# Kernel optimization log

Measured on AMD Instinct MI355X. Metric: run time of the kernel, lower is better.

Reference implementation:

```python
import math
import jax, jax.numpy as jnp
import numpy as np

B, T, D, H, L = 8, 512, 128, 128, 2
W_SCALE = 0.05  # xavier-like small init to keep exp() input gate numerically sane


def setup_inputs() -> dict:
    key = jax.random.key(0)
    ks = jax.random.split(key, 14)
    inp = {"x": jax.random.normal(ks[0], (B, T, D), jnp.float32)}
    names_w = ["Wq", "Wk", "Wv", "Wi", "Wf", "Wo"]
    for j, nm in enumerate(names_w):
        inp[nm] = jax.random.normal(ks[1 + j], (L, H, D), jnp.float32) * W_SCALE
    # q/k/v biases zero-initialized per reset_parameters; gate biases random
    inp["bq"] = jnp.zeros((L, H), jnp.float32)
    inp["bk"] = jnp.zeros((L, H), jnp.float32)
    inp["bv"] = jnp.zeros((L, H), jnp.float32)
    inp["bi"] = jax.random.normal(ks[7], (L, H), jnp.float32) * W_SCALE
    inp["bf"] = jax.random.normal(ks[8], (L, H), jnp.float32) * W_SCALE
    inp["bo"] = jax.random.normal(ks[9], (L, H), jnp.float32) * W_SCALE
    return inp


def _mlstm_layer(xin, Wq, bq, Wk, bk, Wv, bv, Wi, bi, Wf, bf, Wo, bo):
    # xin: (B, T, Din). Precompute all 6 projections for the full sequence.
    q = jnp.einsum("btd,hd->bth", xin, Wq) + bq
    k = (jnp.einsum("btd,hd->bth", xin, Wk) + bk) * (1.0 / math.sqrt(H))
    v = jnp.einsum("btd,hd->bth", xin, Wv) + bv
    i = jnp.exp(jnp.einsum("btd,hd->bth", xin, Wi) + bi)
    f = jax.nn.sigmoid(jnp.einsum("btd,hd->bth", xin, Wf) + bf)
    o = jax.nn.sigmoid(jnp.einsum("btd,hd->bth", xin, Wo) + bo)

    def step(carry, qkvifo):
        C, n = carry                      # C: (B,H,H), n: (B,H)
        qt, kt, vt, it, ft, ot = qkvifo   # each (B,H)
        h_tilde = jnp.einsum("bij,bj->bi", C, qt)
        denom = jnp.maximum(jnp.abs(jnp.einsum("bi,bi->b", n, qt)), 1.0)[:, None]
        h = ot * (h_tilde / denom)
        n_new = ft * n + it * kt
        C_new = ft[:, :, None] * C + it[:, :, None] * (vt[:, :, None] * kt[:, None, :])
        return (C_new, n_new), h

    Bc = xin.shape[0]
    C0 = jnp.zeros((Bc, H, H), xin.dtype)
    n0 = jnp.zeros((Bc, H), xin.dtype)
    seq = tuple(jnp.swapaxes(a, 0, 1) for a in (q, k, v, i, f, o))  # (T,B,H)
    _, hs = jax.lax.scan(step, (C0, n0), seq)
    return jnp.swapaxes(hs, 0, 1)  # (B,T,H)


def reference(x, Wq, bq, Wk, bk, Wv, bv, Wi, bi, Wf, bf, Wo, bo):
    h = x
    for l in range(L):  # small fixed layer loop (dropout=0.0 -> identity)
        h = _mlstm_layer(h, Wq[l], bq[l], Wk[l], bk[l], Wv[l], bv[l],
                         Wi[l], bi[l], Wf[l], bf[l], Wo[l], bo[l])
    return h  # (B, T, H) output sequence of last layer
```

## Files before the change

### kernel.cpp

```cpp
#include <hip/hip_runtime.h>
#include <math.h>

#define BB 8
#define TT 512
#define DD 128
#define HH 128
#define BT_ (BB * TT)
#define CL 64
#define NCH 8
static const size_t BTH = (size_t)BT_ * HH;


struct WArgs { const float* W[6]; };
struct BArgs { const float* b[6]; };

template <int CTRL>
__device__ __forceinline__ float dpp_add(float x) {
  int y = __builtin_amdgcn_update_dpp(0, __builtin_bit_cast(int, x), CTRL,
                                      0xF, 0xF, true);
  return x + __builtin_bit_cast(float, y);
}

template <int CTRL>
__device__ __forceinline__ float dpp_mov(float old, float x) {
  int y = __builtin_amdgcn_update_dpp(__builtin_bit_cast(int, old),
                                      __builtin_bit_cast(int, x), CTRL,
                                      0xF, 0xF, false);
  return __builtin_bit_cast(float, y);
}

__device__ __forceinline__ float rd_lane(float x, int l) {
  return __builtin_bit_cast(
      float, __builtin_amdgcn_readlane(__builtin_bit_cast(int, x), l));
}

__global__ __launch_bounds__(256)
void transpose_w(WArgs w, float* __restrict__ Wt) {
  __shared__ float t[32][33];
  const int l = blockIdx.y / 6, p = blockIdx.y % 6;
  const float* src = w.W[p] + (size_t)l * HH * DD;
  float* dst = Wt + (size_t)blockIdx.y * HH * DD;
  const int ty0 = (blockIdx.x >> 2) * 32, tx0 = (blockIdx.x & 3) * 32;
  const int tx = threadIdx.x & 31, ty = threadIdx.x >> 5;
#pragma unroll
  for (int j = 0; j < 32; j += 8)
    t[ty + j][tx] = src[(size_t)(ty0 + ty + j) * DD + tx0 + tx];
  __syncthreads();
#pragma unroll
  for (int j = 0; j < 32; j += 8)
    dst[(size_t)(tx0 + ty + j) * HH + ty0 + tx] = t[tx][ty + j];
}

__global__ __launch_bounds__(256)
void proj_kernel(const float* __restrict__ X, const float* __restrict__ Wtl,
                 BArgs args, float* __restrict__ act) {
  __shared__ float xs[32][132];
  const int p = blockIdx.y;
  const int row0 = blockIdx.x * 32;
  const int tid = threadIdx.x;
  {
    const float4* xg = (const float4*)(X + (size_t)row0 * DD);
#pragma unroll
    for (int i = 0; i < 4; ++i) {
      int u = tid + 256 * i;
      float4 v = xg[u];
      *(float4*)&xs[u >> 5][(u & 31) * 4] = v;
    }
  }
  __syncthreads();

  const int h0 = (tid & 15) * 8;
  const int r0 = (tid >> 4) * 2;
  const float* wtp = Wtl + (size_t)p * HH * DD;

  float acc[2][8];
#pragma unroll
  for (int r = 0; r < 2; ++r)
#pragma unroll
    for (int j = 0; j < 8; ++j) acc[r][j] = 0.f;

  for (int d0 = 0; d0 < DD; d0 += 4) {
    float4 wa[4], wb[4];
#pragma unroll
    for (int i = 0; i < 4; ++i) {
      wa[i] = *(const float4*)(wtp + (size_t)(d0 + i) * HH + h0);
      wb[i] = *(const float4*)(wtp + (size_t)(d0 + i) * HH + h0 + 4);
    }
    float4 x0 = *(const float4*)&xs[r0][d0];
    float4 x1 = *(const float4*)&xs[r0 + 1][d0];
    const float xa[4] = {x0.x, x0.y, x0.z, x0.w};
    const float xb[4] = {x1.x, x1.y, x1.z, x1.w};
#pragma unroll
    for (int i = 0; i < 4; ++i) {
      acc[0][0] = fmaf(xa[i], wa[i].x, acc[0][0]);
      acc[0][1] = fmaf(xa[i], wa[i].y, acc[0][1]);
      acc[0][2] = fmaf(xa[i], wa[i].z, acc[0][2]);
      acc[0][3] = fmaf(xa[i], wa[i].w, acc[0][3]);
      acc[0][4] = fmaf(xa[i], wb[i].x, acc[0][4]);
      acc[0][5] = fmaf(xa[i], wb[i].y, acc[0][5]);
      acc[0][6] = fmaf(xa[i], wb[i].z, acc[0][6]);
      acc[0][7] = fmaf(xa[i], wb[i].w, acc[0][7]);
      acc[1][0] = fmaf(xb[i], wa[i].x, acc[1][0]);
      acc[1][1] = fmaf(xb[i], wa[i].y, acc[1][1]);
      acc[1][2] = fmaf(xb[i], wa[i].z, acc[1][2]);
      acc[1][3] = fmaf(xb[i], wa[i].w, acc[1][3]);
      acc[1][4] = fmaf(xb[i], wb[i].x, acc[1][4]);
      acc[1][5] = fmaf(xb[i], wb[i].y, acc[1][5]);
      acc[1][6] = fmaf(xb[i], wb[i].z, acc[1][6]);
      acc[1][7] = fmaf(xb[i], wb[i].w, acc[1][7]);
    }
  }

  const float4 b0 = *(const float4*)(args.b[p] + h0);
  const float4 b1 = *(const float4*)(args.b[p] + h0 + 4);
  const float bias[8] = {b0.x, b0.y, b0.z, b0.w, b1.x, b1.y, b1.z, b1.w};
#pragma unroll
  for (int r = 0; r < 2; ++r) {
    const size_t row = (size_t)row0 + r0 + r;
    float v[8];
#pragma unroll
    for (int j = 0; j < 8; ++j) {
      float a = acc[r][j] + bias[j];
      if (p == 1)      a *= 0.088388347648318447f;
      else if (p == 3) a = __expf(a);
      else if (p >= 4) a = 1.0f / (1.0f + __expf(-a));
      v[j] = a;
    }
    if (p == 0) {
      float* dst = act + row * HH + h0;
      *(float4*)dst = make_float4(v[0], v[1], v[2], v[3]);
      *(float4*)(dst + 4) = make_float4(v[4], v[5], v[6], v[7]);
    } else if (p == 1) {
      float* dst = act + BTH + row * HH + h0;
      *(float4*)dst = make_float4(v[0], v[1], v[2], v[3]);
      *(float4*)(dst + 4) = make_float4(v[4], v[5], v[6], v[7]);
    } else if (p == 3 || p == 4) {
      float* dst = act + 2 * BTH + row * 2 * HH + 2 * h0 + (p == 3 ? 0 : 1);
#pragma unroll
      for (int j = 0; j < 8; ++j) dst[2 * j] = v[j];
    } else {
      float* dst = act + 4 * BTH + row * 2 * HH + 2 * h0 + (p == 2 ? 0 : 1);
#pragma unroll
      for (int j = 0; j < 8; ++j) dst[2 * j] = v[j];
    }
  }
}

__global__ __launch_bounds__(128)
void nseg_kernel(const float* __restrict__ act, float* __restrict__ segAB) {
  const int b = blockIdx.x & 7, seg = blockIdx.x >> 3;
  const int p = threadIdx.x;
  const size_t boff = (size_t)b * TT * HH;
  const float* kp = act + BTH + boff + p;
  const float* ifp = act + 2 * BTH + 2 * boff + 2 * p;
  const int t0 = seg * 8;
  float A = 1.f, Bv = 0.f;
#pragma unroll
  for (int j = 0; j < 8; ++j) {
    const float2 iff = *(const float2*)(ifp + (size_t)(t0 + j) * 2 * HH);
    const float kv = kp[(size_t)(t0 + j) * HH];
    A *= iff.y;
    Bv = fmaf(iff.y, Bv, iff.x * kv);
  }
  *(float2*)(segAB + ((size_t)(b * 128 + p) * 64 + seg) * 2) =
      make_float2(A, Bv);
}

__global__ __launch_bounds__(64)
void nsum_kernel(const float* __restrict__ segAB, float* __restrict__ nstart) {
  const int chain = blockIdx.x;
  const int lane = threadIdx.x;
  const float2 ab = *(const float2*)(segAB + ((size_t)chain * 64 + lane) * 2);
  float A = ab.x, Bv = ab.y;
#define SCAN_LVL(CTRL)                          \
  {                                             \
    float As = dpp_mov<CTRL>(1.0f, A);          \
    float Bs = dpp_mov<CTRL>(0.0f, Bv);         \
    Bv = fmaf(A, Bs, Bv);                       \
    A = A * As;                                 \
  }
  SCAN_LVL(0x111)
  SCAN_LVL(0x112)
  SCAN_LVL(0x114)
  SCAN_LVL(0x118)
  SCAN_LVL(0x142)
  SCAN_LVL(0x143)
#undef SCAN_LVL
  const int idx = (lane + 1) & 63;
  nstart[(size_t)chain * 64 + idx] = (lane == 63) ? 0.f : Bv;
}

__global__ __launch_bounds__(128)
void nexp_denom_kernel(float* __restrict__ act,
                       const float* __restrict__ nstart) {
  __shared__ float pl[8][132];
  __shared__ float den[8];
  const int b = blockIdx.x & 7, seg = blockIdx.x >> 3;
  const int p = threadIdx.x;
  const size_t boff = (size_t)b * TT * HH;
  const float* qp = act + boff + p;
  const float* kp = act + BTH + boff + p;
  const float* ifp = act + 2 * BTH + 2 * boff + 2 * p;
  const int t0 = seg * 8;
  float n = nstart[(size_t)(b * 128 + p) * 64 + seg];
  float prod[8];
#pragma unroll
  for (int j = 0; j < 8; ++j) {
    const float2 iff = *(const float2*)(ifp + (size_t)(t0 + j) * 2 * HH);
    const float kv = kp[(size_t)(t0 + j) * HH];
    const float qv = qp[(size_t)(t0 + j) * HH];
    prod[j] = n * qv;
    n = fmaf(iff.y, n, iff.x * kv);
  }
#pragma unroll
  for (int j = 0; j < 8; ++j) pl[j][p] = prod[j];
  __syncthreads();
  {
    const int j = p >> 4, c = p & 15;
    const float4 a = *(const float4*)&pl[j][c * 8];
    const float4 d = *(const float4*)&pl[j][c * 8 + 4];
    float s = ((a.x + a.y) + (a.z + a.w)) + ((d.x + d.y) + (d.z + d.w));
    s = dpp_add<0x111>(s);
    s = dpp_add<0x112>(s);
    s = dpp_add<0x114>(s);
    s = dpp_add<0x118>(s);
    if ((p & 15) == 15)
      den[j] = __builtin_amdgcn_rcpf(fmaxf(fabsf(s), 1.0f));
  }
  __syncthreads();
  float* vop = act + 4 * BTH + 2 * boff;
#pragma unroll
  for (int j = 0; j < 8; ++j)
    vop[(size_t)(t0 + j) * 2 * HH + 2 * p + 1] *= den[j];
}

__global__ __launch_bounds__(512)
void cseg2_kernel(const float* __restrict__ act, float* __restrict__ cbuf,
                  float* __restrict__ abuf) {
  __shared__ __align__(16) float kt[CL][128];
  __shared__ __align__(16) float ift[CL][64];
  __shared__ __align__(16) float vot[CL][64];
  const int tid = threadIdx.x;
  const int lane = tid & 63, wid = tid >> 6;
  const int blk = blockIdx.x;
  const int b = blk & 7, ch = (blk >> 3) & 7, qtr = blk >> 6;
  const int t0 = ch * CL;
  const int p0 = qtr * 32;
  const size_t boff = (size_t)b * TT * HH;
  const float* kg = act + BTH + boff;
  const float* ifg = act + 2 * BTH + 2 * boff;
  const float* vog = act + 4 * BTH + 2 * boff;

#pragma unroll
  for (int i = 0; i < 4; ++i) {
    const int u = tid + 512 * i;
    const int r = u >> 5, c = (u & 31) * 4;
    *(float4*)&kt[r][c] = *(const float4*)(kg + (size_t)(t0 + r) * HH + c);
  }
#pragma unroll
  for (int i = 0; i < 2; ++i) {
    const int u = tid + 512 * i;
    const int r = u >> 4, c = (u & 15) * 4;
    *(float4*)&ift[r][c] =
        *(const float4*)(ifg + (size_t)(t0 + r) * 2 * HH + 2 * p0 + c);
    *(float4*)&vot[r][c] =
        *(const float4*)(vog + (size_t)(t0 + r) * 2 * HH + 2 * p0 + c);
  }
  __syncthreads();

  const int pl = lane >> 4, cl = lane & 15;
  const int plocal = wid * 4 + pl;
  const int p = p0 + plocal;

  float C[8];
#pragma unroll
  for (int j = 0; j < 8; ++j) C[j] = 0.f;
  float Af = 1.f;

#pragma unroll 4
  for (int t = 0; t < CL; ++t) {
    const float2 gif = *(const float2*)&ift[t][2 * plocal];
    const float2 gvo = *(const float2*)&vot[t][2 * plocal];
    const float4 k0 = *(const float4*)&kt[t][cl * 4];
    const float4 k1 = *(const float4*)&kt[t][cl * 4 + 64];
    const float a = gif.x * gvo.x;
    const float f = gif.y;
    C[0] = fmaf(f, C[0], a * k0.x);
    C[1] = fmaf(f, C[1], a * k0.y);
    C[2] = fmaf(f, C[2], a * k0.z);
    C[3] = fmaf(f, C[3], a * k0.w);
    C[4] = fmaf(f, C[4], a * k1.x);
    C[5] = fmaf(f, C[5], a * k1.y);
    C[6] = fmaf(f, C[6], a * k1.z);
    C[7] = fmaf(f, C[7], a * k1.w);
    Af *= f;
  }

  const size_t slot = (size_t)(b * 128 + p) * NCH + ch;
  *(float4*)(cbuf + slot * 128 + cl * 4) = make_float4(C[0], C[1], C[2], C[3]);
  *(float4*)(cbuf + slot * 128 + cl * 4 + 64) =
      make_float4(C[4], C[5], C[6], C[7]);
  if (cl == 0) abuf[slot] = Af;
}

__global__ __launch_bounds__(64)
void ccomb_kernel(float* __restrict__ cbuf, const float* __restrict__ abuf) {
  const int chain = blockIdx.x;
  const int lane = threadIdx.x;
  const float av = abuf[(size_t)chain * 8 + (lane & 7)];
  float Cs0 = 0.f, Cs1 = 0.f;
#pragma unroll
  for (int g = 0; g < 8; ++g) {
    float* ptr = cbuf + ((size_t)chain * 8 + g) * 128 + 2 * lane;
    const float2 Bv = *(const float2*)ptr;
    const float Ag = rd_lane(av, g);
    *(float2*)ptr = make_float2(Cs0, Cs1);
    Cs0 = fmaf(Ag, Cs0, Bv.x);
    Cs1 = fmaf(Ag, Cs1, Bv.y);
  }
}

__global__ __launch_bounds__(512)
void hscan2_kernel(const float* __restrict__ act, float* __restrict__ hout,
                   const float* __restrict__ cbuf) {
  __shared__ __align__(16) float qt[CL][128];
  __shared__ __align__(16) float kt[CL][128];
  __shared__ __align__(16) float ift[CL][64];
  __shared__ __align__(16) float vot[CL][64];
  const int tid = threadIdx.x;
  const int lane = tid & 63, wid = tid >> 6;
  const int blk = blockIdx.x;
  const int b = blk & 7, ch = (blk >> 3) & 7, qtr = blk >> 6;
  const int t0 = ch * CL;
  const int p0 = qtr * 32;
  const size_t boff = (size_t)b * TT * HH;
  const float* qg = act + boff;
  const float* kg = act + BTH + boff;
  const float* ifg = act + 2 * BTH + 2 * boff;
  const float* vog = act + 4 * BTH + 2 * boff;

#pragma unroll
  for (int i = 0; i < 4; ++i) {
    const int u = tid + 512 * i;
    const int r = u >> 5, c = (u & 31) * 4;
    *(float4*)&qt[r][c] = *(const float4*)(qg + (size_t)(t0 + r) * HH + c);
    *(float4*)&kt[r][c] = *(const float4*)(kg + (size_t)(t0 + r) * HH + c);
  }
#pragma unroll
  for (int i = 0; i < 2; ++i) {
    const int u = tid + 512 * i;
    const int r = u >> 4, c = (u & 15) * 4;
    *(float4*)&ift[r][c] =
        *(const float4*)(ifg + (size_t)(t0 + r) * 2 * HH + 2 * p0 + c);
    *(float4*)&vot[r][c] =
        *(const float4*)(vog + (size_t)(t0 + r) * 2 * HH + 2 * p0 + c);
  }
  __syncthreads();

  const int pl = lane >> 4, cl = lane & 15;
  const int plocal = wid * 4 + pl;
  const int p = p0 + plocal;

  float C[8];
  {
    const size_t slot = (size_t)(b * 128 + p) * NCH + ch;
    const float4 c0 = *(const float4*)(cbuf + slot * 128 + cl * 4);
    const float4 c1 = *(const float4*)(cbuf + slot * 128 + cl * 4 + 64);
    C[0] = c0.x; C[1] = c0.y; C[2] = c0.z; C[3] = c0.w;
    C[4] = c1.x; C[5] = c1.y; C[6] = c1.z; C[7] = c1.w;
  }
  float* hbase = hout + boff + p;

#pragma unroll 4
  for (int t = 0; t < CL; ++t) {
    const float2 gif = *(const float2*)&ift[t][2 * plocal];
    const float2 gvo = *(const float2*)&vot[t][2 * plocal];
    const float4 q0 = *(const float4*)&qt[t][cl * 4];
    const float4 q1 = *(const float4*)&qt[t][cl * 4 + 64];
    const float4 k0 = *(const float4*)&kt[t][cl * 4];
    const float4 k1 = *(const float4*)&kt[t][cl * 4 + 64];
    float s0 = C[0] * q0.x;
    float s1 = C[4] * q1.x;
    s0 = fmaf(C[1], q0.y, s0);
    s1 = fmaf(C[5], q1.y, s1);
    s0 = fmaf(C[2], q0.z, s0);
    s1 = fmaf(C[6], q1.z, s1);
    s0 = fmaf(C[3], q0.w, s0);
    s1 = fmaf(C[7], q1.w, s1);
    float s = s0 + s1;
    const float a = gif.x * gvo.x;
    const float f = gif.y;
    C[0] = fmaf(f, C[0], a * k0.x);
    C[1] = fmaf(f, C[1], a * k0.y);
    C[2] = fmaf(f, C[2], a * k0.z);
    C[3] = fmaf(f, C[3], a * k0.w);
    C[4] = fmaf(f, C[4], a * k1.x);
    C[5] = fmaf(f, C[5], a * k1.y);
    C[6] = fmaf(f, C[6], a * k1.z);
    C[7] = fmaf(f, C[7], a * k1.w);
    s = dpp_add<0x111>(s);
    s = dpp_add<0x112>(s);
    s = dpp_add<0x114>(s);
    s = dpp_add<0x118>(s);
    if (cl == 15) hbase[(size_t)(t0 + t) * HH] = s * gvo.y;
  }
}

extern "C" void kernel_launch(void* const* d_in, const int* in_sizes, int n_in,
                              void* d_out, int out_size, void* d_ws,
                              size_t ws_size, hipStream_t stream) {
  (void)in_sizes; (void)n_in; (void)out_size; (void)ws_size;
  const float* x = (const float*)d_in[0];
  float* act = (float*)d_ws;
  float* hbuf = act + 6 * BTH;
  float* cbuf = act + 7 * BTH;
  float* abuf = cbuf + (size_t)1024 * 8 * 128;
  float* Wt = (float*)d_out;
  float* segAB = Wt + 196608;
  float* nstart = Wt + 327680;

  WArgs wa;
  for (int j = 0; j < 6; ++j) wa.W[j] = (const float*)d_in[1 + j];
  transpose_w<<<dim3(16, 12), 256, 0, stream>>>(wa, Wt);

  for (int l = 0; l < 2; ++l) {
    BArgs ba;
    for (int j = 0; j < 6; ++j)
      ba.b[j] = (const float*)d_in[7 + j] + (size_t)l * HH;
    const float* wtl = Wt + (size_t)l * 6 * HH * DD;
    const float* xin = (l == 0) ? x : hbuf;
    float* hdst = (l == 0) ? hbuf : (float*)d_out;
    proj_kernel<<<dim3(BT_ / 32, 6), 256, 0, stream>>>(xin, wtl, ba, act);
    nseg_kernel<<<512, 128, 0, stream>>>(act, segAB);
    nsum_kernel<<<1024, 64, 0, stream>>>(segAB, nstart);
    nexp_denom_kernel<<<512, 128, 0, stream>>>(act, nstart);
    cseg2_kernel<<<256, 512, 0, stream>>>(act, cbuf, abuf);
    ccomb_kernel<<<1024, 64, 0, stream>>>(cbuf, abuf);
    hscan2_kernel<<<256, 512, 0, stream>>>(act, hdst, cbuf);
  }
}
```

Measured before the change: 220.5 us.

## Fold normalizer scan into chunk pass and inline cross-chunk state combine

Halves the chunk length so the chunk-local C and hidden-state scans launch twice as many blocks. The n-state chunk summary is computed inside the C-chunk kernel, and a single ndenom kernel combines the chunk prefixes and computes the denominators, replacing three separate n kernels. The ccomb kernel is dropped: each hscan block rebuilds its starting C by serially folding all earlier chunk states. This cuts launches per layer from six to three, at the cost of redundant prefix work that grows with chunk index and a low-parallelism ndenom kernel with serial loops.

```diff
diff --git a/kernel.cpp b/kernel.cpp
--- a/kernel.cpp
+++ b/kernel.cpp
@@ -6,8 +6,8 @@
 #define DD 128
 #define HH 128
 #define BT_ (BB * TT)
-#define CL 64
-#define NCH 8
+#define CL 32
+#define NCH 16
 static const size_t BTH = (size_t)BT_ * HH;
 
 
@@ -19,19 +19,6 @@
   int y = __builtin_amdgcn_update_dpp(0, __builtin_bit_cast(int, x), CTRL,
                                       0xF, 0xF, true);
   return x + __builtin_bit_cast(float, y);
-}
-
-template <int CTRL>
-__device__ __forceinline__ float dpp_mov(float old, float x) {
-  int y = __builtin_amdgcn_update_dpp(__builtin_bit_cast(int, old),
-                                      __builtin_bit_cast(int, x), CTRL,
-                                      0xF, 0xF, false);
-  return __builtin_bit_cast(float, y);
-}
-
-__device__ __forceinline__ float rd_lane(float x, int l) {
-  return __builtin_bit_cast(
-      float, __builtin_amdgcn_readlane(__builtin_bit_cast(int, x), l));
 }
 
 __global__ __launch_bounds__(256)
@@ -146,104 +133,16 @@
   }
 }
 
-__global__ __launch_bounds__(128)
-void nseg_kernel(const float* __restrict__ act, float* __restrict__ segAB) {
-  const int b = blockIdx.x & 7, seg = blockIdx.x >> 3;
-  const int p = threadIdx.x;
-  const size_t boff = (size_t)b * TT * HH;
-  const float* kp = act + BTH + boff + p;
-  const float* ifp = act + 2 * BTH + 2 * boff + 2 * p;
-  const int t0 = seg * 8;
-  float A = 1.f, Bv = 0.f;
-#pragma unroll
-  for (int j = 0; j < 8; ++j) {
-    const float2 iff = *(const float2*)(ifp + (size_t)(t0 + j) * 2 * HH);
-    const float kv = kp[(size_t)(t0 + j) * HH];
-    A *= iff.y;
-    Bv = fmaf(iff.y, Bv, iff.x * kv);
-  }
-  *(float2*)(segAB + ((size_t)(b * 128 + p) * 64 + seg) * 2) =
-      make_float2(A, Bv);
-}
-
-__global__ __launch_bounds__(64)
-void nsum_kernel(const float* __restrict__ segAB, float* __restrict__ nstart) {
-  const int chain = blockIdx.x;
-  const int lane = threadIdx.x;
-  const float2 ab = *(const float2*)(segAB + ((size_t)chain * 64 + lane) * 2);
-  float A = ab.x, Bv = ab.y;
-#define SCAN_LVL(CTRL)                          \
-  {                                             \
-    float As = dpp_mov<CTRL>(1.0f, A);          \
-    float Bs = dpp_mov<CTRL>(0.0f, Bv);         \
-    Bv = fmaf(A, Bs, Bv);                       \
-    A = A * As;                                 \
-  }
-  SCAN_LVL(0x111)
-  SCAN_LVL(0x112)
-  SCAN_LVL(0x114)
-  SCAN_LVL(0x118)
-  SCAN_LVL(0x142)
-  SCAN_LVL(0x143)
-#undef SCAN_LVL
-  const int idx = (lane + 1) & 63;
-  nstart[(size_t)chain * 64 + idx] = (lane == 63) ? 0.f : Bv;
-}
-
-__global__ __launch_bounds__(128)
-void nexp_denom_kernel(float* __restrict__ act,
-                       const float* __restrict__ nstart) {
-  __shared__ float pl[8][132];
-  __shared__ float den[8];
-  const int b = blockIdx.x & 7, seg = blockIdx.x >> 3;
-  const int p = threadIdx.x;
-  const size_t boff = (size_t)b * TT * HH;
-  const float* qp = act + boff + p;
-  const float* kp = act + BTH + boff + p;
-  const float* ifp = act + 2 * BTH + 2 * boff + 2 * p;
-  const int t0 = seg * 8;
-  float n = nstart[(size_t)(b * 128 + p) * 64 + seg];
-  float prod[8];
-#pragma unroll
-  for (int j = 0; j < 8; ++j) {
-    const float2 iff = *(const float2*)(ifp + (size_t)(t0 + j) * 2 * HH);
-    const float kv = kp[(size_t)(t0 + j) * HH];
-    const float qv = qp[(size_t)(t0 + j) * HH];
-    prod[j] = n * qv;
-    n = fmaf(iff.y, n, iff.x * kv);
-  }
-#pragma unroll
-  for (int j = 0; j < 8; ++j) pl[j][p] = prod[j];
-  __syncthreads();
-  {
-    const int j = p >> 4, c = p & 15;
-    const float4 a = *(const float4*)&pl[j][c * 8];
-    const float4 d = *(const float4*)&pl[j][c * 8 + 4];
-    float s = ((a.x + a.y) + (a.z + a.w)) + ((d.x + d.y) + (d.z + d.w));
-    s = dpp_add<0x111>(s);
-    s = dpp_add<0x112>(s);
-    s = dpp_add<0x114>(s);
-    s = dpp_add<0x118>(s);
-    if ((p & 15) == 15)
-      den[j] = __builtin_amdgcn_rcpf(fmaxf(fabsf(s), 1.0f));
-  }
-  __syncthreads();
-  float* vop = act + 4 * BTH + 2 * boff;
-#pragma unroll
-  for (int j = 0; j < 8; ++j)
-    vop[(size_t)(t0 + j) * 2 * HH + 2 * p + 1] *= den[j];
-}
-
 __global__ __launch_bounds__(512)
 void cseg2_kernel(const float* __restrict__ act, float* __restrict__ cbuf,
-                  float* __restrict__ abuf) {
+                  float* __restrict__ abuf, float* __restrict__ nbufB) {
   __shared__ __align__(16) float kt[CL][128];
   __shared__ __align__(16) float ift[CL][64];
   __shared__ __align__(16) float vot[CL][64];
   const int tid = threadIdx.x;
   const int lane = tid & 63, wid = tid >> 6;
   const int blk = blockIdx.x;
-  const int b = blk & 7, ch = (blk >> 3) & 7, qtr = blk >> 6;
+  const int b = blk & 7, ch = (blk >> 3) & (NCH - 1), qtr = blk >> 7;
   const int t0 = ch * CL;
   const int p0 = qtr * 32;
   const size_t boff = (size_t)b * TT * HH;
@@ -252,15 +151,13 @@
   const float* vog = act + 4 * BTH + 2 * boff;
 
 #pragma unroll
-  for (int i = 0; i < 4; ++i) {
+  for (int i = 0; i < CL / 16; ++i) {
     const int u = tid + 512 * i;
     const int r = u >> 5, c = (u & 31) * 4;
     *(float4*)&kt[r][c] = *(const float4*)(kg + (size_t)(t0 + r) * HH + c);
   }
-#pragma unroll
-  for (int i = 0; i < 2; ++i) {
-    const int u = tid + 512 * i;
-    const int r = u >> 4, c = (u & 15) * 4;
+  {
+    const int r = tid >> 4, c = (tid & 15) * 4;
     *(float4*)&ift[r][c] =
         *(const float4*)(ifg + (size_t)(t0 + r) * 2 * HH + 2 * p0 + c);
     *(float4*)&vot[r][c] =
@@ -275,7 +172,7 @@
   float C[8];
 #pragma unroll
   for (int j = 0; j < 8; ++j) C[j] = 0.f;
-  float Af = 1.f;
+  float Af = 1.f, Bn = 0.f;
 
 #pragma unroll 4
   for (int t = 0; t < CL; ++t) {
@@ -283,6 +180,7 @@
     const float2 gvo = *(const float2*)&vot[t][2 * plocal];
     const float4 k0 = *(const float4*)&kt[t][cl * 4];
     const float4 k1 = *(const float4*)&kt[t][cl * 4 + 64];
+    const float kp = kt[t][p];
     const float a = gif.x * gvo.x;
     const float f = gif.y;
     C[0] = fmaf(f, C[0], a * k0.x);
@@ -294,35 +192,75 @@
     C[6] = fmaf(f, C[6], a * k1.z);
     C[7] = fmaf(f, C[7], a * k1.w);
     Af *= f;
+    Bn = fmaf(f, Bn, gif.x * kp);
   }
 
   const size_t slot = (size_t)(b * 128 + p) * NCH + ch;
   *(float4*)(cbuf + slot * 128 + cl * 4) = make_float4(C[0], C[1], C[2], C[3]);
   *(float4*)(cbuf + slot * 128 + cl * 4 + 64) =
       make_float4(C[4], C[5], C[6], C[7]);
-  if (cl == 0) abuf[slot] = Af;
-}
-
-__global__ __launch_bounds__(64)
-void ccomb_kernel(float* __restrict__ cbuf, const float* __restrict__ abuf) {
-  const int chain = blockIdx.x;
-  const int lane = threadIdx.x;
-  const float av = abuf[(size_t)chain * 8 + (lane & 7)];
-  float Cs0 = 0.f, Cs1 = 0.f;
-#pragma unroll
-  for (int g = 0; g < 8; ++g) {
-    float* ptr = cbuf + ((size_t)chain * 8 + g) * 128 + 2 * lane;
-    const float2 Bv = *(const float2*)ptr;
-    const float Ag = rd_lane(av, g);
-    *(float2*)ptr = make_float2(Cs0, Cs1);
-    Cs0 = fmaf(Ag, Cs0, Bv.x);
-    Cs1 = fmaf(Ag, Cs1, Bv.y);
+  if (cl == 0) {
+    abuf[slot] = Af;
+    nbufB[slot] = Bn;
+  }
+}
+
+__global__ __launch_bounds__(128)
+void ndenom_kernel(float* __restrict__ act, const float* __restrict__ abuf,
+                   const float* __restrict__ nbufB) {
+  __shared__ float plds[8][132];
+  __shared__ float den[8];
+  const int b = blockIdx.x & 7, ch = blockIdx.x >> 3;
+  const int p = threadIdx.x;
+  const size_t boff = (size_t)b * TT * HH;
+  const float* qp = act + boff + p;
+  const float* kp = act + BTH + boff + p;
+  const float* ifp = act + 2 * BTH + 2 * boff + 2 * p;
+  float* vop = act + 4 * BTH + 2 * boff;
+  const size_t cb = (size_t)(b * 128 + p) * NCH;
+
+  float n = 0.f;
+#pragma unroll 1
+  for (int g = 0; g < ch; ++g) n = fmaf(abuf[cb + g], n, nbufB[cb + g]);
+
+#pragma unroll 1
+  for (int grp = 0; grp < CL / 8; ++grp) {
+    const int t0 = ch * CL + grp * 8;
+    float prod[8];
+#pragma unroll
+    for (int j = 0; j < 8; ++j) {
+      const float2 iff = *(const float2*)(ifp + (size_t)(t0 + j) * 2 * HH);
+      const float kv = kp[(size_t)(t0 + j) * HH];
+      const float qv = qp[(size_t)(t0 + j) * HH];
+      prod[j] = n * qv;
+      n = fmaf(iff.y, n, iff.x * kv);
+    }
+#pragma unroll
+    for (int j = 0; j < 8; ++j) plds[j][p] = prod[j];
+    __syncthreads();
+    {
+      const int j = p >> 4, c = p & 15;
+      const float4 a = *(const float4*)&plds[j][c * 8];
+      const float4 d = *(const float4*)&plds[j][c * 8 + 4];
+      float s = ((a.x + a.y) + (a.z + a.w)) + ((d.x + d.y) + (d.z + d.w));
+      s = dpp_add<0x111>(s);
+      s = dpp_add<0x112>(s);
+      s = dpp_add<0x114>(s);
+      s = dpp_add<0x118>(s);
+      if ((p & 15) == 15)
+        den[j] = __builtin_amdgcn_rcpf(fmaxf(fabsf(s), 1.0f));
+    }
+    __syncthreads();
+#pragma unroll
+    for (int j = 0; j < 8; ++j)
+      vop[(size_t)(t0 + j) * 2 * HH + 2 * p + 1] *= den[j];
   }
 }
 
 __global__ __launch_bounds__(512)
 void hscan2_kernel(const float* __restrict__ act, float* __restrict__ hout,
-                   const float* __restrict__ cbuf) {
+                   const float* __restrict__ cbuf,
+                   const float* __restrict__ abuf) {
   __shared__ __align__(16) float qt[CL][128];
   __shared__ __align__(16) float kt[CL][128];
   __shared__ __align__(16) float ift[CL][64];
@@ -330,7 +268,7 @@
   const int tid = threadIdx.x;
   const int lane = tid & 63, wid = tid >> 6;
   const int blk = blockIdx.x;
-  const int b = blk & 7, ch = (blk >> 3) & 7, qtr = blk >> 6;
+  const int b = blk & 7, ch = (blk >> 3) & (NCH - 1), qtr = blk >> 7;
   const int t0 = ch * CL;
   const int p0 = qtr * 32;
   const size_t boff = (size_t)b * TT * HH;
@@ -340,16 +278,14 @@
   const float* vog = act + 4 * BTH + 2 * boff;
 
 #pragma unroll
-  for (int i = 0; i < 4; ++i) {
+  for (int i = 0; i < CL / 16; ++i) {
     const int u = tid + 512 * i;
     const int r = u >> 5, c = (u & 31) * 4;
     *(float4*)&qt[r][c] = *(const float4*)(qg + (size_t)(t0 + r) * HH + c);
     *(float4*)&kt[r][c] = *(const float4*)(kg + (size_t)(t0 + r) * HH + c);
   }
-#pragma unroll
-  for (int i = 0; i < 2; ++i) {
-    const int u = tid + 512 * i;
-    const int r = u >> 4, c = (u & 15) * 4;
+  {
+    const int r = tid >> 4, c = (tid & 15) * 4;
     *(float4*)&ift[r][c] =
         *(const float4*)(ifg + (size_t)(t0 + r) * 2 * HH + 2 * p0 + c);
     *(float4*)&vot[r][c] =
@@ -362,12 +298,24 @@
   const int p = p0 + plocal;
 
   float C[8];
+#pragma unroll
+  for (int j = 0; j < 8; ++j) C[j] = 0.f;
   {
-    const size_t slot = (size_t)(b * 128 + p) * NCH + ch;
-    const float4 c0 = *(const float4*)(cbuf + slot * 128 + cl * 4);
-    const float4 c1 = *(const float4*)(cbuf + slot * 128 + cl * 4 + 64);
-    C[0] = c0.x; C[1] = c0.y; C[2] = c0.z; C[3] = c0.w;
-    C[4] = c1.x; C[5] = c1.y; C[6] = c1.z; C[7] = c1.w;
+    const size_t cb = (size_t)(b * 128 + p) * NCH;
+#pragma unroll 1
+    for (int g = 0; g < ch; ++g) {
+      const float a = abuf[cb + g];
+      const float4 b0 = *(const float4*)(cbuf + (cb + g) * 128 + cl * 4);
+      const float4 b1 = *(const float4*)(cbuf + (cb + g) * 128 + cl * 4 + 64);
+      C[0] = fmaf(a, C[0], b0.x);
+      C[1] = fmaf(a, C[1], b0.y);
+      C[2] = fmaf(a, C[2], b0.z);
+      C[3] = fmaf(a, C[3], b0.w);
+      C[4] = fmaf(a, C[4], b1.x);
+      C[5] = fmaf(a, C[5], b1.y);
+      C[6] = fmaf(a, C[6], b1.z);
+      C[7] = fmaf(a, C[7], b1.w);
+    }
   }
   float* hbase = hout + boff + p;
 
@@ -414,10 +362,9 @@
   float* act = (float*)d_ws;
   float* hbuf = act + 6 * BTH;
   float* cbuf = act + 7 * BTH;
-  float* abuf = cbuf + (size_t)1024 * 8 * 128;
+  float* abuf = cbuf + (size_t)1024 * NCH * 128;
+  float* nbufB = abuf + (size_t)1024 * NCH;
   float* Wt = (float*)d_out;
-  float* segAB = Wt + 196608;
-  float* nstart = Wt + 327680;
 
   WArgs wa;
   for (int j = 0; j < 6; ++j) wa.W[j] = (const float*)d_in[1 + j];
@@ -431,11 +378,8 @@
     const float* xin = (l == 0) ? x : hbuf;
     float* hdst = (l == 0) ? hbuf : (float*)d_out;
     proj_kernel<<<dim3(BT_ / 32, 6), 256, 0, stream>>>(xin, wtl, ba, act);
-    nseg_kernel<<<512, 128, 0, stream>>>(act, segAB);
-    nsum_kernel<<<1024, 64, 0, stream>>>(segAB, nstart);
-    nexp_denom_kernel<<<512, 128, 0, stream>>>(act, nstart);
-    cseg2_kernel<<<256, 512, 0, stream>>>(act, cbuf, abuf);
-    ccomb_kernel<<<1024, 64, 0, stream>>>(cbuf, abuf);
-    hscan2_kernel<<<256, 512, 0, stream>>>(act, hdst, cbuf);
-  }
-}
+    cseg2_kernel<<<512, 512, 0, stream>>>(act, cbuf, abuf, nbufB);
+    ndenom_kernel<<<128, 128, 0, stream>>>(act, abuf, nbufB);
+    hscan2_kernel<<<512, 512, 0, stream>>>(act, hdst, cbuf, abuf);
+  }
+}
```

After: 216.7 us. Within noise of the previous version (-1.7%).
